# Kernel optimization log

Hardware: AMD Instinct MI355X
Metric: run time of the kernel (lower is better)

The kernel has to match this reference:

```python
import jax, jax.numpy as jnp
import numpy as np

B, N, M = 64, 1024, 80
C1, D = 288, 256  # object_dim, lang_dim
EPS = 1e-12  # F.normalize eps


def setup_inputs() -> dict:
    key = jax.random.key(0)
    ks = jax.random.split(key, 16)
    w = lambda k, s: jax.random.normal(k, s, jnp.float32) * 0.05
    object_feat = jax.random.normal(ks[0], (B, N, C1), jnp.float32)
    lang_feat = jax.random.normal(ks[1], (B, M, D), jnp.float32)
    lang_mask = jax.random.randint(ks[2], (B, M), 0, 2).astype(jnp.int32)
    lang_mask = lang_mask.at[:, 0].set(1)  # ensure >=1 valid token per row
    return {
        "object_feat": object_feat,
        "lang_feat": lang_feat,
        "lang_mask": lang_mask,
        # object_att_fc: Linear(C1,D) -> ReLU -> Linear(D,D)
        "W1": w(ks[3], (C1, D)), "b1": w(ks[4], (D,)),
        "W2": w(ks[5], (D, D)), "b2": w(ks[6], (D,)),
        # atten_fc: Dropout(eval=identity) -> Linear(2D,1)
        "Wa": w(ks[7], (2 * D, 1)), "ba": w(ks[8], (1,)),
        # object_score_fc: Linear(C1,D) -> ReLU -> Linear(D,D)
        "W3": w(ks[9], (C1, D)), "b3": w(ks[10], (D,)),
        "W4": w(ks[11], (D, D)), "b4": w(ks[12], (D,)),
        # score_fc: Dropout(eval=identity) -> Linear(D,1)
        "Ws": w(ks[13], (D, 1)), "bs": w(ks[14], (1,)),
    }


def reference(object_feat, lang_feat, lang_mask, W1, b1, W2, b2, Wa, ba, W3, b3, W4, b4, Ws, bs):
    # object attention features: (B,N,D)
    oa = jnp.maximum(object_feat @ W1 + b1, 0.0) @ W2 + b2
    # additive attention: cat([oa, lang]) @ Wa == oa @ Wa[:D] + lang @ Wa[D:]
    w_o, w_l = Wa[:D, 0], Wa[D:, 0]
    score = (oa @ w_o)[:, :, None] + (lang_feat @ w_l)[:, None, :] + ba[0]  # (B,N,M)
    score = jnp.where(lang_mask[:, None, :] == 0, -jnp.inf, score)
    att = jax.nn.softmax(score, axis=2)  # (B,N,M)
    att_feat = jnp.einsum("bnm,bmd->bnd", att, lang_feat)  # sum(att * lang_att)
    # object score branch
    osc = jnp.maximum(object_feat @ W3 + b3, 0.0) @ W4 + b4  # (B,N,D)
    x = jnp.maximum(att_feat * osc, 0.0)
    # F.normalize over channel dim (dim=2)
    nrm = jnp.sqrt(jnp.sum(x * x, axis=2, keepdims=True))
    x = x / jnp.maximum(nrm, EPS)
    out = x @ Ws + bs  # (B,N,1)
    return jnp.transpose(out, (0, 2, 1))  # (B,1,N)
```

## Files before the change

kernel.cpp:

```cpp
#include <hip/hip_runtime.h>
#include <math.h>
#include <stdint.h>

#define B_  64
#define N_  1024
#define M_  80
#define C1_ 288
#define D_  256
#define EPS_ 1e-12f

typedef _Float16 f16;
typedef _Float16 f16x8 __attribute__((ext_vector_type(8)));
typedef float    f32x4 __attribute__((ext_vector_type(4)));

#define ATT_OFF 0
#define W3F_OFF 65536
#define W4F_OFF (65536 + 147456)
#define H3_OFF  (65536 + 147456 + 131072)

__device__ __forceinline__ void g2l16(const void* g, void* l) {
    __builtin_amdgcn_global_load_lds(
        (const __attribute__((address_space(1))) uint32_t*)g,
        (__attribute__((address_space(3))) uint32_t*)l, 16, 0, 0);
}

__global__ __launch_bounds__(256) void prep_kernel(
    const float* __restrict__ lang_feat,
    const int*   __restrict__ lang_mask,
    const float* __restrict__ Wa,
    const float* __restrict__ W3,
    const float* __restrict__ W4,
    float* __restrict__ att_ws,
    f16* __restrict__ w3f, f16* __restrict__ w4f)
{
    const int bi = blockIdx.x;
    if (bi >= B_) {
        const int kb = bi - B_;
        const float* src; f16* dst; int K0;
        if (kb < 9) { src = W3; dst = w3f + kb * 8192;       K0 = kb * 32; }
        else        { src = W4; dst = w4f + (kb - 9) * 8192; K0 = (kb - 9) * 32; }
        for (int idx = threadIdx.x; idx < 8192; idx += 256) {
            int nt  = idx >> 9;
            int rem = idx & 511;
            int ln  = rem >> 3;
            int i   = rem & 7;
            int k   = K0 + ((ln >> 4) << 3) + i;
            int col = (nt << 4) + (ln & 15);
            dst[idx] = (f16)src[k * D_ + col];
        }
        return;
    }

    __shared__ float wl_s[D_];
    __shared__ float ls[M_];
    const int b   = bi;
    const int tid = threadIdx.x;

    wl_s[tid] = Wa[D_ + tid];
    __syncthreads();

    const int wave = tid >> 6, lane = tid & 63;
    for (int m = wave; m < M_; m += 4) {
        const float* lf = lang_feat + (size_t)(b * M_ + m) * D_;
        float p = 0.f;
        #pragma unroll
        for (int j = 0; j < 4; ++j) { int d = lane + 64 * j; p = fmaf(lf[d], wl_s[d], p); }
        #pragma unroll
        for (int off = 32; off; off >>= 1) p += __shfl_xor(p, off);
        if (lane == 0) ls[m] = (lang_mask[b * M_ + m] == 0) ? -INFINITY : p;
    }
    __syncthreads();

    float mx = -INFINITY;
    #pragma unroll
    for (int m0 = 0; m0 < M_; m0 += 8) {
        float v0 = ls[m0], v1 = ls[m0+1], v2 = ls[m0+2], v3 = ls[m0+3];
        float v4 = ls[m0+4], v5 = ls[m0+5], v6 = ls[m0+6], v7 = ls[m0+7];
        mx = fmaxf(mx, fmaxf(fmaxf(fmaxf(v0,v1), fmaxf(v2,v3)),
                             fmaxf(fmaxf(v4,v5), fmaxf(v6,v7))));
    }
    __syncthreads();
    if (tid < M_) ls[tid] = expf(ls[tid] - mx);
    __syncthreads();

    float s0 = 0.f, s1 = 0.f, s2 = 0.f, s3 = 0.f;
    #pragma unroll
    for (int m0 = 0; m0 < M_; m0 += 8) {
        s0 += ls[m0] + ls[m0+4];
        s1 += ls[m0+1] + ls[m0+5];
        s2 += ls[m0+2] + ls[m0+6];
        s3 += ls[m0+3] + ls[m0+7];
    }
    const float inv = 1.f / ((s0 + s1) + (s2 + s3));

    const int d = tid;
    float a0 = 0.f, a1 = 0.f, a2 = 0.f, a3 = 0.f;
    const float* lfb = lang_feat + (size_t)b * M_ * D_ + d;
    #pragma unroll 5
    for (int m = 0; m < M_; m += 4) {
        a0 = fmaf(ls[m],   lfb[(size_t)m * D_],       a0);
        a1 = fmaf(ls[m+1], lfb[(size_t)(m+1) * D_],   a1);
        a2 = fmaf(ls[m+2], lfb[(size_t)(m+2) * D_],   a2);
        a3 = fmaf(ls[m+3], lfb[(size_t)(m+3) * D_],   a3);
    }
    att_ws[b * D_ + d] = ((a0 + a1) + (a2 + a3)) * inv;
}

__global__ __launch_bounds__(512, 2) void gemm1_kernel(
    const float* __restrict__ obj,
    const f16*  __restrict__ w3f,
    const float* __restrict__ b3,
    f16* __restrict__ h3)
{
    extern __shared__ char smem[];
    const int tid  = threadIdx.x;
    const int lane = tid & 63;
    const int w    = tid >> 6;

    #pragma unroll
    for (int i = 0; i < 18; ++i) {
        int off = (i * 512 + tid) * 16;
        g2l16((const char*)w3f + off, smem + off);
    }
    __syncthreads();

    const int r0   = (blockIdx.x * 8 + w) * 32;
    const int colc = lane & 15;
    const int kc   = (lane >> 4) << 3;

    f32x4 acc0[16], acc1[16];
    #pragma unroll
    for (int nt = 0; nt < 16; ++nt) {
        float bv = b3[(nt << 4) + colc];
        acc0[nt] = (f32x4){bv, bv, bv, bv};
        acc1[nt] = acc0[nt];
    }

    const float* arow0 = obj + (size_t)(r0 + colc) * C1_ + kc;
    const float* arow1 = arow0 + 16 * C1_;

    #pragma unroll 3
    for (int ks = 0; ks < 9; ++ks) {
        float4 p00 = *(const float4*)(arow0 + ks * 32);
        float4 p01 = *(const float4*)(arow0 + ks * 32 + 4);
        float4 p10 = *(const float4*)(arow1 + ks * 32);
        float4 p11 = *(const float4*)(arow1 + ks * 32 + 4);
        f16x8 a0 = {(f16)p00.x,(f16)p00.y,(f16)p00.z,(f16)p00.w,
                    (f16)p01.x,(f16)p01.y,(f16)p01.z,(f16)p01.w};
        f16x8 a1 = {(f16)p10.x,(f16)p10.y,(f16)p10.z,(f16)p10.w,
                    (f16)p11.x,(f16)p11.y,(f16)p11.z,(f16)p11.w};
        const char* bb = smem + ks * 16384;
        #pragma unroll
        for (int nt = 0; nt < 16; ++nt) {
            f16x8 bf = *(const f16x8*)&bb[nt * 1024 + lane * 16];
            acc0[nt] = __builtin_amdgcn_mfma_f32_16x16x32_f16(a0, bf, acc0[nt], 0, 0, 0);
            acc1[nt] = __builtin_amdgcn_mfma_f32_16x16x32_f16(a1, bf, acc1[nt], 0, 0, 0);
        }
    }

    const int rbase = (lane >> 4) << 2;
    #pragma unroll
    for (int h = 0; h < 2; ++h) {
        #pragma unroll
        for (int r = 0; r < 4; ++r) {
            int row = r0 + 16 * h + rbase + r;
            f16* dst = h3 + (size_t)row * D_ + colc;
            #pragma unroll
            for (int nt = 0; nt < 16; ++nt) {
                f32x4 a = h ? acc1[nt] : acc0[nt];
                dst[nt << 4] = (f16)fmaxf(a[r], 0.f);
            }
        }
    }
}

__global__ __launch_bounds__(512, 2) void gemm2_kernel(
    const f16*  __restrict__ h3,
    const f16*  __restrict__ w4f,
    const float* __restrict__ b4,
    const float* __restrict__ Ws,
    const float* __restrict__ bs,
    const float* __restrict__ att,
    float* __restrict__ out)
{
    extern __shared__ char smem[];
    const int tid  = threadIdx.x;
    const int lane = tid & 63;
    const int w    = tid >> 6;

    #pragma unroll
    for (int i = 0; i < 16; ++i) {
        int off = (i * 512 + tid) * 16;
        g2l16((const char*)w4f + off, smem + off);
    }
    __syncthreads();

    const int r0   = (blockIdx.x * 8 + w) * 32;
    const int b    = r0 >> 10;
    const int colc = lane & 15;
    const int kcB  = (lane >> 4) << 3;

    f32x4 acc0[16], acc1[16];
    #pragma unroll
    for (int nt = 0; nt < 16; ++nt) {
        float bv = b4[(nt << 4) + colc];
        acc0[nt] = (f32x4){bv, bv, bv, bv};
        acc1[nt] = acc0[nt];
    }

    const f16* a0p = h3 + (size_t)(r0 + colc) * D_ + kcB;
    const f16* a1p = a0p + 16 * D_;

    #pragma unroll 4
    for (int ks = 0; ks < 8; ++ks) {
        f16x8 a0 = *(const f16x8*)(a0p + ks * 32);
        f16x8 a1 = *(const f16x8*)(a1p + ks * 32);
        const char* bb = smem + ks * 16384;
        #pragma unroll
        for (int nt = 0; nt < 16; ++nt) {
            f16x8 bf = *(const f16x8*)&bb[nt * 1024 + lane * 16];
            acc0[nt] = __builtin_amdgcn_mfma_f32_16x16x32_f16(a0, bf, acc0[nt], 0, 0, 0);
            acc1[nt] = __builtin_amdgcn_mfma_f32_16x16x32_f16(a1, bf, acc1[nt], 0, 0, 0);
        }
    }

    const float bsv = bs[0];
    float s20[4] = {0,0,0,0}, sw0[4] = {0,0,0,0};
    float s21[4] = {0,0,0,0}, sw1[4] = {0,0,0,0};
    #pragma unroll
    for (int nt = 0; nt < 16; ++nt) {
        int colg = (nt << 4) + colc;
        float av = att[(b << 8) + colg];
        float wv = Ws[colg];
        #pragma unroll
        for (int r = 0; r < 4; ++r) {
            float x0 = fmaxf(av * acc0[nt][r], 0.f);
            float x1 = fmaxf(av * acc1[nt][r], 0.f);
            s20[r] = fmaf(x0, x0, s20[r]);  sw0[r] = fmaf(x0, wv, sw0[r]);
            s21[r] = fmaf(x1, x1, s21[r]);  sw1[r] = fmaf(x1, wv, sw1[r]);
        }
    }
    #pragma unroll
    for (int off = 1; off < 16; off <<= 1) {
        #pragma unroll
        for (int r = 0; r < 4; ++r) {
            s20[r] += __shfl_xor(s20[r], off);  sw0[r] += __shfl_xor(sw0[r], off);
            s21[r] += __shfl_xor(s21[r], off);  sw1[r] += __shfl_xor(sw1[r], off);
        }
    }
    if (colc == 0) {
        const int rbase = (lane >> 4) << 2;
        #pragma unroll
        for (int r = 0; r < 4; ++r) {
            out[r0 + rbase + r]      = sw0[r] / fmaxf(sqrtf(s20[r]), EPS_) + bsv;
            out[r0 + 16 + rbase + r] = sw1[r] / fmaxf(sqrtf(s21[r]), EPS_) + bsv;
        }
    }
}

extern "C" void kernel_launch(void* const* d_in, const int* in_sizes, int n_in,
                              void* d_out, int out_size, void* d_ws, size_t ws_size,
                              hipStream_t stream) {
    const float* object_feat = (const float*)d_in[0];
    const float* lang_feat   = (const float*)d_in[1];
    const int*   lang_mask   = (const int*)d_in[2];
    const float* Wa = (const float*)d_in[7];
    const float* W3 = (const float*)d_in[9];
    const float* b3 = (const float*)d_in[10];
    const float* W4 = (const float*)d_in[11];
    const float* b4 = (const float*)d_in[12];
    const float* Ws = (const float*)d_in[13];
    const float* bs = (const float*)d_in[14];
    float* out = (float*)d_out;

    char* ws   = (char*)d_ws;
    float* att = (float*)(ws + ATT_OFF);
    f16*  w3f  = (f16*)(ws + W3F_OFF);
    f16*  w4f  = (f16*)(ws + W4F_OFF);
    f16*  h3   = (f16*)(ws + H3_OFF);

    hipFuncSetAttribute(reinterpret_cast<const void*>(gemm1_kernel),
                        hipFuncAttributeMaxDynamicSharedMemorySize, 147456);
    hipFuncSetAttribute(reinterpret_cast<const void*>(gemm2_kernel),
                        hipFuncAttributeMaxDynamicSharedMemorySize, 131072);

    prep_kernel<<<B_ + 17, 256, 0, stream>>>(lang_feat, lang_mask, Wa, W3, W4,
                                             att, w3f, w4f);
    gemm1_kernel<<<256, 512, 147456, stream>>>(object_feat, w3f, b3, h3);
    gemm2_kernel<<<256, 512, 131072, stream>>>(h3, w4f, b4, Ws, bs, att, out);
}
```

Before: 171.6 us.

## Fuse both MLP GEMMs into one kernel, keeping hidden activations in registers

Merges the two GEMM kernels into one. The first layer's output stays in registers and is rearranged across lanes with ds_bpermute to form the A operand of the second MFMA, so the fp16 h3 round trip through global memory and one kernel launch are removed. W3 is now read straight from global/L2 instead of being staged in LDS, and the MFMA operands are swapped so results come out transposed. The cost is higher register pressure, permute overhead, and global loads of W3 inside the inner loop.

```diff
diff --git a/kernel.cpp b/kernel.cpp
--- a/kernel.cpp
+++ b/kernel.cpp
@@ -16,12 +16,24 @@
 #define ATT_OFF 0
 #define W3F_OFF 65536
 #define W4F_OFF (65536 + 147456)
-#define H3_OFF  (65536 + 147456 + 131072)
 
 __device__ __forceinline__ void g2l16(const void* g, void* l) {
     __builtin_amdgcn_global_load_lds(
         (const __attribute__((address_space(1))) uint32_t*)g,
         (__attribute__((address_space(3))) uint32_t*)l, 16, 0, 0);
+}
+
+__device__ __forceinline__ uint32_t pk2(float a, float b) {
+    union { f16 h[2]; uint32_t u; } c;
+    c.h[0] = (f16)a; c.h[1] = (f16)b;
+    return c.u;
+}
+
+__device__ __forceinline__ f16x8 w4_to_f16x8(uint32_t w0, uint32_t w1,
+                                             uint32_t w2, uint32_t w3) {
+    union { uint32_t u[4]; f16x8 h; } c;
+    c.u[0] = w0; c.u[1] = w1; c.u[2] = w2; c.u[3] = w3;
+    return c.h;
 }
 
 __global__ __launch_bounds__(256) void prep_kernel(
@@ -106,77 +118,11 @@
     att_ws[b * D_ + d] = ((a0 + a1) + (a2 + a3)) * inv;
 }
 
-__global__ __launch_bounds__(512, 2) void gemm1_kernel(
+__global__ __launch_bounds__(512, 2) void main_kernel(
     const float* __restrict__ obj,
     const f16*  __restrict__ w3f,
+    const f16*  __restrict__ w4f,
     const float* __restrict__ b3,
-    f16* __restrict__ h3)
-{
-    extern __shared__ char smem[];
-    const int tid  = threadIdx.x;
-    const int lane = tid & 63;
-    const int w    = tid >> 6;
-
-    #pragma unroll
-    for (int i = 0; i < 18; ++i) {
-        int off = (i * 512 + tid) * 16;
-        g2l16((const char*)w3f + off, smem + off);
-    }
-    __syncthreads();
-
-    const int r0   = (blockIdx.x * 8 + w) * 32;
-    const int colc = lane & 15;
-    const int kc   = (lane >> 4) << 3;
-
-    f32x4 acc0[16], acc1[16];
-    #pragma unroll
-    for (int nt = 0; nt < 16; ++nt) {
-        float bv = b3[(nt << 4) + colc];
-        acc0[nt] = (f32x4){bv, bv, bv, bv};
-        acc1[nt] = acc0[nt];
-    }
-
-    const float* arow0 = obj + (size_t)(r0 + colc) * C1_ + kc;
-    const float* arow1 = arow0 + 16 * C1_;
-
-    #pragma unroll 3
-    for (int ks = 0; ks < 9; ++ks) {
-        float4 p00 = *(const float4*)(arow0 + ks * 32);
-        float4 p01 = *(const float4*)(arow0 + ks * 32 + 4);
-        float4 p10 = *(const float4*)(arow1 + ks * 32);
-        float4 p11 = *(const float4*)(arow1 + ks * 32 + 4);
-        f16x8 a0 = {(f16)p00.x,(f16)p00.y,(f16)p00.z,(f16)p00.w,
-                    (f16)p01.x,(f16)p01.y,(f16)p01.z,(f16)p01.w};
-        f16x8 a1 = {(f16)p10.x,(f16)p10.y,(f16)p10.z,(f16)p10.w,
-                    (f16)p11.x,(f16)p11.y,(f16)p11.z,(f16)p11.w};
-        const char* bb = smem + ks * 16384;
-        #pragma unroll
-        for (int nt = 0; nt < 16; ++nt) {
-            f16x8 bf = *(const f16x8*)&bb[nt * 1024 + lane * 16];
-            acc0[nt] = __builtin_amdgcn_mfma_f32_16x16x32_f16(a0, bf, acc0[nt], 0, 0, 0);
-            acc1[nt] = __builtin_amdgcn_mfma_f32_16x16x32_f16(a1, bf, acc1[nt], 0, 0, 0);
-        }
-    }
-
-    const int rbase = (lane >> 4) << 2;
-    #pragma unroll
-    for (int h = 0; h < 2; ++h) {
-        #pragma unroll
-        for (int r = 0; r < 4; ++r) {
-            int row = r0 + 16 * h + rbase + r;
-            f16* dst = h3 + (size_t)row * D_ + colc;
-            #pragma unroll
-            for (int nt = 0; nt < 16; ++nt) {
-                f32x4 a = h ? acc1[nt] : acc0[nt];
-                dst[nt << 4] = (f16)fmaxf(a[r], 0.f);
-            }
-        }
-    }
-}
-
-__global__ __launch_bounds__(512, 2) void gemm2_kernel(
-    const f16*  __restrict__ h3,
-    const f16*  __restrict__ w4f,
     const float* __restrict__ b4,
     const float* __restrict__ Ws,
     const float* __restrict__ bs,
@@ -187,74 +133,118 @@
     const int tid  = threadIdx.x;
     const int lane = tid & 63;
     const int w    = tid >> 6;
+    const int g    = lane & 15;
+    const int q    = lane >> 4;
 
     #pragma unroll
     for (int i = 0; i < 16; ++i) {
         int off = (i * 512 + tid) * 16;
         g2l16((const char*)w4f + off, smem + off);
     }
-    __syncthreads();
-
-    const int r0   = (blockIdx.x * 8 + w) * 32;
-    const int b    = r0 >> 10;
-    const int colc = lane & 15;
-    const int kcB  = (lane >> 4) << 3;
-
-    f32x4 acc0[16], acc1[16];
+
+    const int r0w = (blockIdx.x * 8 + w) * 32;
+    const int b   = blockIdx.x >> 2;
+
+    f32x4 acc[2][16];
     #pragma unroll
     for (int nt = 0; nt < 16; ++nt) {
-        float bv = b4[(nt << 4) + colc];
-        acc0[nt] = (f32x4){bv, bv, bv, bv};
-        acc1[nt] = acc0[nt];
-    }
-
-    const f16* a0p = h3 + (size_t)(r0 + colc) * D_ + kcB;
-    const f16* a1p = a0p + 16 * D_;
-
-    #pragma unroll 4
+        f32x4 bv = *(const f32x4*)&b3[nt * 16 + q * 4];
+        acc[0][nt] = bv; acc[1][nt] = bv;
+    }
+
+    const float* ap0 = obj + (size_t)(r0w + g) * C1_ + q * 8;
+    const float* ap1 = ap0 + 16 * C1_;
+
+    #pragma unroll 3
+    for (int ks = 0; ks < 9; ++ks) {
+        float4 p00 = *(const float4*)(ap0 + ks * 32);
+        float4 p01 = *(const float4*)(ap0 + ks * 32 + 4);
+        float4 p10 = *(const float4*)(ap1 + ks * 32);
+        float4 p11 = *(const float4*)(ap1 + ks * 32 + 4);
+        f16x8 o0 = {(f16)p00.x,(f16)p00.y,(f16)p00.z,(f16)p00.w,
+                    (f16)p01.x,(f16)p01.y,(f16)p01.z,(f16)p01.w};
+        f16x8 o1 = {(f16)p10.x,(f16)p10.y,(f16)p10.z,(f16)p10.w,
+                    (f16)p11.x,(f16)p11.y,(f16)p11.z,(f16)p11.w};
+        const f16* wp = w3f + ks * 8192;
+        #pragma unroll
+        for (int nt = 0; nt < 16; ++nt) {
+            f16x8 wf = *(const f16x8*)(wp + nt * 512 + lane * 8);
+            acc[0][nt] = __builtin_amdgcn_mfma_f32_16x16x32_f16(wf, o0, acc[0][nt], 0, 0, 0);
+            acc[1][nt] = __builtin_amdgcn_mfma_f32_16x16x32_f16(wf, o1, acc[1][nt], 0, 0, 0);
+        }
+    }
+
+    uint32_t S[2][16][2];
+    #pragma unroll
+    for (int h = 0; h < 2; ++h)
+        #pragma unroll
+        for (int nt = 0; nt < 16; ++nt) {
+            S[h][nt][0] = pk2(fmaxf(acc[h][nt][0], 0.f), fmaxf(acc[h][nt][1], 0.f));
+            S[h][nt][1] = pk2(fmaxf(acc[h][nt][2], 0.f), fmaxf(acc[h][nt][3], 0.f));
+        }
+
+    const int a0 = (g + 32 * (q & 1)) * 4;
+    const int a1 = a0 + 64;
+    const bool hi = (lane >= 32);
+    f16x8 hf[2][8];
+    #pragma unroll
+    for (int h = 0; h < 2; ++h)
+        #pragma unroll
+        for (int ks = 0; ks < 8; ++ks) {
+            uint32_t wd[4];
+            #pragma unroll
+            for (int p = 0; p < 4; ++p) {
+                int ad = (p >> 1) ? a1 : a0;
+                int vA = __builtin_amdgcn_ds_bpermute(ad, (int)S[h][2*ks][p & 1]);
+                int vB = __builtin_amdgcn_ds_bpermute(ad, (int)S[h][2*ks+1][p & 1]);
+                wd[p] = hi ? (uint32_t)vB : (uint32_t)vA;
+            }
+            hf[h][ks] = w4_to_f16x8(wd[0], wd[1], wd[2], wd[3]);
+        }
+
+    f32x4 acc2[2][16];
+    #pragma unroll
+    for (int nt = 0; nt < 16; ++nt) {
+        f32x4 bv = *(const f32x4*)&b4[nt * 16 + q * 4];
+        acc2[0][nt] = bv; acc2[1][nt] = bv;
+    }
+
+    __syncthreads();
+
+    #pragma unroll
     for (int ks = 0; ks < 8; ++ks) {
-        f16x8 a0 = *(const f16x8*)(a0p + ks * 32);
-        f16x8 a1 = *(const f16x8*)(a1p + ks * 32);
-        const char* bb = smem + ks * 16384;
+        const char* bp = smem + ks * 16384;
         #pragma unroll
         for (int nt = 0; nt < 16; ++nt) {
-            f16x8 bf = *(const f16x8*)&bb[nt * 1024 + lane * 16];
-            acc0[nt] = __builtin_amdgcn_mfma_f32_16x16x32_f16(a0, bf, acc0[nt], 0, 0, 0);
-            acc1[nt] = __builtin_amdgcn_mfma_f32_16x16x32_f16(a1, bf, acc1[nt], 0, 0, 0);
+            f16x8 wf = *(const f16x8*)&bp[nt * 1024 + lane * 16];
+            acc2[0][nt] = __builtin_amdgcn_mfma_f32_16x16x32_f16(wf, hf[0][ks], acc2[0][nt], 0, 0, 0);
+            acc2[1][nt] = __builtin_amdgcn_mfma_f32_16x16x32_f16(wf, hf[1][ks], acc2[1][nt], 0, 0, 0);
         }
     }
 
     const float bsv = bs[0];
-    float s20[4] = {0,0,0,0}, sw0[4] = {0,0,0,0};
-    float s21[4] = {0,0,0,0}, sw1[4] = {0,0,0,0};
+    float s2[2] = {0.f, 0.f}, sw[2] = {0.f, 0.f};
     #pragma unroll
     for (int nt = 0; nt < 16; ++nt) {
-        int colg = (nt << 4) + colc;
-        float av = att[(b << 8) + colg];
-        float wv = Ws[colg];
-        #pragma unroll
-        for (int r = 0; r < 4; ++r) {
-            float x0 = fmaxf(av * acc0[nt][r], 0.f);
-            float x1 = fmaxf(av * acc1[nt][r], 0.f);
-            s20[r] = fmaf(x0, x0, s20[r]);  sw0[r] = fmaf(x0, wv, sw0[r]);
-            s21[r] = fmaf(x1, x1, s21[r]);  sw1[r] = fmaf(x1, wv, sw1[r]);
-        }
-    }
-    #pragma unroll
-    for (int off = 1; off < 16; off <<= 1) {
-        #pragma unroll
-        for (int r = 0; r < 4; ++r) {
-            s20[r] += __shfl_xor(s20[r], off);  sw0[r] += __shfl_xor(sw0[r], off);
-            s21[r] += __shfl_xor(s21[r], off);  sw1[r] += __shfl_xor(sw1[r], off);
-        }
-    }
-    if (colc == 0) {
-        const int rbase = (lane >> 4) << 2;
-        #pragma unroll
-        for (int r = 0; r < 4; ++r) {
-            out[r0 + rbase + r]      = sw0[r] / fmaxf(sqrtf(s20[r]), EPS_) + bsv;
-            out[r0 + 16 + rbase + r] = sw1[r] / fmaxf(sqrtf(s21[r]), EPS_) + bsv;
-        }
+        f32x4 av = *(const f32x4*)&att[(b << 8) + nt * 16 + q * 4];
+        f32x4 wv = *(const f32x4*)&Ws[nt * 16 + q * 4];
+        #pragma unroll
+        for (int h = 0; h < 2; ++h)
+            #pragma unroll
+            for (int r = 0; r < 4; ++r) {
+                float x = fmaxf(av[r] * acc2[h][nt][r], 0.f);
+                s2[h] = fmaf(x, x, s2[h]);
+                sw[h] = fmaf(x, wv[r], sw[h]);
+            }
+    }
+    #pragma unroll
+    for (int h = 0; h < 2; ++h) {
+        s2[h] += __shfl_xor(s2[h], 16);  sw[h] += __shfl_xor(sw[h], 16);
+        s2[h] += __shfl_xor(s2[h], 32);  sw[h] += __shfl_xor(sw[h], 32);
+    }
+    if (lane < 16) {
+        out[r0w + g]      = sw[0] / fmaxf(sqrtf(s2[0]), EPS_) + bsv;
+        out[r0w + 16 + g] = sw[1] / fmaxf(sqrtf(s2[1]), EPS_) + bsv;
     }
 }
 
@@ -277,15 +267,12 @@
     float* att = (float*)(ws + ATT_OFF);
     f16*  w3f  = (f16*)(ws + W3F_OFF);
     f16*  w4f  = (f16*)(ws + W4F_OFF);
-    f16*  h3   = (f16*)(ws + H3_OFF);
-
-    hipFuncSetAttribute(reinterpret_cast<const void*>(gemm1_kernel),
-                        hipFuncAttributeMaxDynamicSharedMemorySize, 147456);
-    hipFuncSetAttribute(reinterpret_cast<const void*>(gemm2_kernel),
+
+    hipFuncSetAttribute(reinterpret_cast<const void*>(main_kernel),
                         hipFuncAttributeMaxDynamicSharedMemorySize, 131072);
 
     prep_kernel<<<B_ + 17, 256, 0, stream>>>(lang_feat, lang_mask, Wa, W3, W4,
                                              att, w3f, w4f);
-    gemm1_kernel<<<256, 512, 147456, stream>>>(object_feat, w3f, b3, h3);
-    gemm2_kernel<<<256, 512, 131072, stream>>>(h3, w4f, b4, Ws, bs, att, out);
-}
+    main_kernel<<<256, 512, 131072, stream>>>(object_feat, w3f, w4f,
+                                              b3, b4, Ws, bs, att, out);
+}
```

After: 174.5 us. Within noise of the previous version (+1.7%).
